# Performance work log

Hardware: AMD Instinct MI355X
Metric: run time of the kernel (lower is better)

The kernel has to match this reference:

```python
import jax, jax.numpy as jnp
import numpy as np

B, S, D, H = 2, 2048, 1024, 16
HD = D // H

def setup_inputs() -> dict:
    key = jax.random.key(0)
    ks = jax.random.split(key, 5)
    x = jax.random.normal(ks[0], (B, S, D), dtype=jnp.float32)
    scale = float(np.sqrt(6.0 / (D + D)))  # xavier_uniform bound
    def xavier(k):
        return jax.random.uniform(k, (D, D), dtype=jnp.float32, minval=-scale, maxval=scale)
    WQ, WK, WV, WO = xavier(ks[1]), xavier(ks[2]), xavier(ks[3]), xavier(ks[4])
    # causal mask, 1 = valid, 0 = masked, shape (B, 1, S_q, S_k)
    mask = jnp.broadcast_to(jnp.tril(jnp.ones((S, S), dtype=jnp.int32)), (B, 1, S, S))
    return {"x": x, "WQ": WQ, "WK": WK, "WV": WV, "WO": WO, "mask": mask}

def reference(x, WQ, WK, WV, WO, mask):
    b, s, d = x.shape
    # projections and head split: (B, H, S, HD)
    def split_heads(t):
        return t.reshape(b, s, H, HD).transpose(0, 2, 1, 3)
    q = split_heads(x @ WQ)
    k = split_heads(x @ WK)
    v = split_heads(x @ WV)
    scores = jnp.einsum('bhqd,bhkd->bhqk', q, k) / jnp.sqrt(jnp.float32(HD))
    neg = jnp.finfo(scores.dtype).min
    scores = jnp.where(mask == 0, neg, scores)
    attn = jax.nn.softmax(scores, axis=-1)
    out = jnp.einsum('bhqk,bhkd->bhqd', attn, v)  # (B, H, S, HD)
    out = out.transpose(0, 2, 1, 3).reshape(b, s, d)
    return out @ WO
```

## Files before the change

### kernel.cpp

```cpp
#include <hip/hip_runtime.h>
#include <hip/hip_bf16.h>


typedef __attribute__((ext_vector_type(8))) short short8;
typedef __attribute__((ext_vector_type(4))) float floatx4;
typedef __attribute__((ext_vector_type(4))) unsigned short ushort4v;
typedef __attribute__((ext_vector_type(2))) unsigned int uint2v;

#define GLDS16(gp, lp) __builtin_amdgcn_global_load_lds( \
    (const __attribute__((address_space(1))) void*)(gp), \
    (__attribute__((address_space(3))) void*)(lp), 16, 0, 0)

#define EXP2F(x) __builtin_amdgcn_exp2f(x)
#define NEG_INF (-__builtin_inff())

__device__ __forceinline__ unsigned short f2bf(float f) {
  unsigned int u = __builtin_bit_cast(unsigned int, f);
  return (unsigned short)((u + 0x7fffu + ((u >> 16) & 1u)) >> 16);
}
__device__ __forceinline__ float bf2f(unsigned short h) {
  unsigned int u = ((unsigned int)h) << 16;
  return __builtin_bit_cast(float, u);
}
__device__ __forceinline__ unsigned int pack2bf(float a, float b) {
#if __has_builtin(__builtin_amdgcn_cvt_pk_bf16_f32)
  auto r = __builtin_amdgcn_cvt_pk_bf16_f32(a, b);
  return __builtin_bit_cast(unsigned int, r);
#else
  unsigned int ua = (__builtin_bit_cast(unsigned int, a) + 0x8000u) >> 16;
  unsigned int ub = (__builtin_bit_cast(unsigned int, b) + 0x8000u) & 0xFFFF0000u;
  return ua | ub;
#endif
}
__device__ __forceinline__ floatx4 mfma16(short8 a, short8 b, floatx4 c) {
  return __builtin_amdgcn_mfma_f32_16x16x32_bf16(a, b, c, 0, 0, 0);
}

__global__ void k_convert_x(const float* __restrict__ x, unsigned short* __restrict__ xb) {
  int i = (blockIdx.x * 256 + threadIdx.x) * 4;
  ushort4v o;
  o.x = f2bf(x[i + 0]);
  o.y = f2bf(x[i + 1]);
  o.z = f2bf(x[i + 2]);
  o.w = f2bf(x[i + 3]);
  *(ushort4v*)(xb + i) = o;
}

__global__ void k_transpose_w(const float* __restrict__ WQ, const float* __restrict__ WK,
                              const float* __restrict__ WV, const float* __restrict__ WO,
                              unsigned short* __restrict__ wtq, unsigned short* __restrict__ wto,
                              int* __restrict__ counter) {
  if (threadIdx.x == 0 && blockIdx.x == 0 && blockIdx.y == 0 && blockIdx.z == 0) *counter = 0;
  __shared__ float tile[32][33];
  const float* W = (blockIdx.z == 0) ? WQ : (blockIdx.z == 1) ? WK : (blockIdx.z == 2) ? WV : WO;
  unsigned short* dst = (blockIdx.z < 3) ? (wtq + (size_t)blockIdx.z * 1024 * 1024) : wto;
  int tx = threadIdx.x & 31, ty = threadIdx.x >> 5;
  int bx = blockIdx.x, by = blockIdx.y;
#pragma unroll
  for (int j = 0; j < 4; ++j)
    tile[ty + j * 8][tx] = W[(size_t)(by * 32 + ty + j * 8) * 1024 + bx * 32 + tx];
  __syncthreads();
#pragma unroll
  for (int j = 0; j < 4; ++j)
    dst[(size_t)(bx * 32 + ty + j * 8) * 1024 + by * 32 + tx] = f2bf(tile[tx][ty + j * 8]);
}

template <int MODE>
__global__ __launch_bounds__(256, 2) void k_gemm(
    const unsigned short* __restrict__ A, const unsigned short* __restrict__ BT,
    float* __restrict__ Cf, unsigned short* __restrict__ Qp,
    unsigned short* __restrict__ Kp, unsigned short* __restrict__ Vt, int K) {
  __shared__ __align__(16) unsigned short smem[128 * 136];
  unsigned short* lA = smem;
  unsigned short* lB = smem + 128 * 64;
  const int tid = threadIdx.x;
  const int wave = tid >> 6, lane = tid & 63;
  const int wm = wave & 1, wn = wave >> 1;
  const int m0 = blockIdx.x * 128, n0 = blockIdx.y * 128;
  const int l15 = lane & 15, l16 = lane >> 4;
  const int r8 = lane >> 3, c8 = lane & 7;
  const int gchunk = (c8 ^ r8) << 3;

  floatx4 acc[4][4] = {};
  for (int k0 = 0; k0 < K; k0 += 64) {
    __syncthreads();
#pragma unroll
    for (int i = 0; i < 4; ++i) {
      int seg = wave * 4 + i;
      int row = seg * 8 + r8;
      GLDS16(A + (size_t)(m0 + row) * K + k0 + gchunk, lA + seg * 512);
      GLDS16(BT + (size_t)(n0 + row) * K + k0 + gchunk, lB + seg * 512);
    }
    __syncthreads();
#pragma unroll
    for (int ks = 0; ks < 2; ++ks) {
      short8 af[4], bfr[4];
#pragma unroll
      for (int t = 0; t < 4; ++t) {
        int m = wm * 64 + t * 16 + l15;
        int cl = ks * 4 + l16;
        af[t] = *(const short8*)(lA + m * 64 + ((cl ^ (m & 7)) << 3));
        int n = wn * 64 + t * 16 + l15;
        bfr[t] = *(const short8*)(lB + n * 64 + ((cl ^ (n & 7)) << 3));
      }
#pragma unroll
      for (int mt = 0; mt < 4; ++mt)
#pragma unroll
        for (int nt = 0; nt < 4; ++nt)
          acc[mt][nt] = mfma16(af[mt], bfr[nt], acc[mt][nt]);
    }
  }
  const int sel = n0 >> 10;
  if (MODE == 1) {
#pragma unroll
    for (int mt = 0; mt < 4; ++mt)
#pragma unroll
      for (int nt = 0; nt < 4; ++nt)
#pragma unroll
        for (int r = 0; r < 4; ++r) {
          int m = m0 + wm * 64 + mt * 16 + l16 * 4 + r;
          int n = n0 + wn * 64 + nt * 16 + l15;
          Cf[(size_t)m * 1024 + n] = acc[mt][nt][r];
        }
  } else if (sel < 2) {
    unsigned short* dst = (sel == 0) ? Qp : Kp;
    __syncthreads();
#pragma unroll
    for (int mt = 0; mt < 4; ++mt)
#pragma unroll
      for (int nt = 0; nt < 4; ++nt)
#pragma unroll
        for (int r = 0; r < 4; ++r) {
          int ml = wm * 64 + mt * 16 + l16 * 4 + r;
          int nl = wn * 64 + nt * 16 + l15;
          smem[ml * 136 + nl] = f2bf(acc[mt][nt][r]);
        }
    __syncthreads();
    const int b = m0 >> 11, s0 = m0 & 2047;
    const int h0 = (n0 & 1023) >> 6;
#pragma unroll
    for (int it = 0; it < 8; ++it) {
      int ml = it * 16 + (tid >> 4);
      int c = (tid & 15) * 8;
      short8 v = *(const short8*)(smem + ml * 136 + c);
      int h = h0 + (c >> 6), hd = c & 63;
      *(short8*)(dst + ((size_t)((b * 16 + h) * 2048 + s0 + ml) << 6) + hd) = v;
    }
  } else {
    __syncthreads();
#pragma unroll
    for (int mt = 0; mt < 4; ++mt)
#pragma unroll
      for (int nt = 0; nt < 4; ++nt)
#pragma unroll
        for (int r = 0; r < 4; ++r) {
          int nl = wn * 64 + nt * 16 + l15;
          int ml = wm * 64 + mt * 16 + l16 * 4 + r;
          smem[nl * 136 + ml] = f2bf(acc[mt][nt][r]);
        }
    __syncthreads();
    const int b = m0 >> 11, s0 = m0 & 2047;
    const int h0 = (n0 - 2048) >> 6;
#pragma unroll
    for (int it = 0; it < 8; ++it) {
      int nl = it * 16 + (tid >> 4);
      int sc = (tid & 15) * 8;
      short8 v = *(const short8*)(smem + nl * 136 + sc);
      int hh = h0 + (nl >> 6), hd = nl & 63;
      *(short8*)(Vt + ((size_t)(b * 16 + hh) * 64 + hd) * 2048 + s0 + sc) = v;
    }
  }
}

__global__ __launch_bounds__(256, 2) void k_attn(
    const unsigned short* __restrict__ Qp, const unsigned short* __restrict__ Kp,
    const unsigned short* __restrict__ Vt, float* __restrict__ Opart,
    float* __restrict__ lpart, int* __restrict__ counter) {
  __shared__ __align__(16) unsigned short kvbuf[2][2][64 * 64];
  __shared__ __align__(16) unsigned short pbuf[4][32 * 64];
  __shared__ int sjob;
  const int tid = threadIdx.x, wave = tid >> 6, lane = tid & 63;
  const int l15 = lane & 15, l16 = lane >> 4;
  const int r8 = lane >> 3, c8 = lane & 7;
  const int gchunk = (c8 ^ r8) << 3;
  unsigned short* pb = &pbuf[wave][0];
  const float qscale = 0.125f * 1.44269504088896f;
  short8 onesv;
#pragma unroll
  for (int j = 0; j < 8; ++j) onesv[j] = (short)0x3F80;

#define STAGE(KT, BUF) \
  { _Pragma("unroll") for (int i_ = 0; i_ < 2; ++i_) { \
      int seg_ = wave * 2 + i_; \
      GLDS16(Kp + base + (size_t)((KT) * 64 + seg_ * 8 + r8) * 64 + gchunk, \
             &kvbuf[BUF][0][0] + seg_ * 512); \
      GLDS16(Vt + base + (size_t)(seg_ * 8 + r8) * 2048 + (KT) * 64 + gchunk, \
             &kvbuf[BUF][1][0] + seg_ * 512); \
    } }

  for (;;) {
    __syncthreads();
    if (tid == 0) sjob = atomicAdd(counter, 1);
    __syncthreads();
    const int job = sjob;
    if (job >= 1024) break;
    const int qt = 15 - (job >> 6);
    const int half = (job >> 5) & 1;
    const int bh = job & 31;
    const int kt0 = half ? (qt + 1) : 0;
    const int kt1 = half ? (2 * qt + 2) : (qt + 1);
    const int R0 = qt * 128 + wave * 32;
    const size_t base = (size_t)bh << 17;

    short8 qf[2][2];
#pragma unroll
    for (int mt = 0; mt < 2; ++mt)
#pragma unroll
      for (int ks = 0; ks < 2; ++ks) {
        short8 v = *(const short8*)(Qp + base + (size_t)(R0 + mt * 16 + l15) * 64 +
                                    ks * 32 + l16 * 8);
#pragma unroll
        for (int j = 0; j < 8; ++j) {
          float f = bf2f((unsigned short)v[j]) * qscale;
          v[j] = (short)f2bf(f);
        }
        qf[mt][ks] = v;
      }

    floatx4 oacc[4][2] = {};
    floatx4 lacc[2] = {};

    STAGE(kt0, 0);
    for (int kt = kt0; kt < kt1; ++kt) {
      const int cb = (kt - kt0) & 1;
      __syncthreads();
      if (kt + 1 < kt1) STAGE(kt + 1, cb ^ 1);
      if (kt * 64 > R0 + 31) continue;
      const unsigned short* kb = &kvbuf[cb][0][0];
      const unsigned short* vb = &kvbuf[cb][1][0];

      floatx4 sacc[2][4] = {};
#pragma unroll
      for (int ks = 0; ks < 2; ++ks) {
        short8 kfr[4];
#pragma unroll
        for (int nt = 0; nt < 4; ++nt) {
          int row = nt * 16 + l15;
          int cl = ks * 4 + l16;
          kfr[nt] = *(const short8*)(kb + row * 64 + ((cl ^ (row & 7)) << 3));
        }
#pragma unroll
        for (int mt = 0; mt < 2; ++mt)
#pragma unroll
          for (int nt = 0; nt < 4; ++nt)
            sacc[mt][nt] = mfma16(kfr[nt], qf[mt][ks], sacc[mt][nt]);
      }
      if (kt * 64 + 63 > R0) {
#pragma unroll
        for (int mt = 0; mt < 2; ++mt)
#pragma unroll
          for (int nt = 0; nt < 4; ++nt)
#pragma unroll
            for (int rr = 0; rr < 4; ++rr) {
              int key = kt * 64 + nt * 16 + l16 * 4 + rr;
              int qrow = R0 + mt * 16 + l15;
              if (key > qrow) sacc[mt][nt][rr] = NEG_INF;
            }
      }
#pragma unroll
      for (int mt = 0; mt < 2; ++mt)
#pragma unroll
        for (int nt = 0; nt < 4; ++nt) {
          uint2v pk;
          pk.x = pack2bf(EXP2F(sacc[mt][nt][0]), EXP2F(sacc[mt][nt][1]));
          pk.y = pack2bf(EXP2F(sacc[mt][nt][2]), EXP2F(sacc[mt][nt][3]));
          int q = mt * 16 + l15;
          int ch = (nt * 4 + l16) ^ ((q & 7) << 1);
          *(uint2v*)(pb + q * 64 + ch * 4) = pk;
        }
      short8 pfr[2][2];
#pragma unroll
      for (int mt = 0; mt < 2; ++mt)
#pragma unroll
        for (int ks = 0; ks < 2; ++ks) {
          int q = mt * 16 + l15;
          int ch = (ks * 8 + l16 * 2) ^ ((q & 7) << 1);
          pfr[mt][ks] = *(const short8*)(pb + q * 64 + ch * 4);
        }
#pragma unroll
      for (int ks = 0; ks < 2; ++ks) {
        short8 vf[4];
#pragma unroll
        for (int ht = 0; ht < 4; ++ht) {
          int row = ht * 16 + l15;
          int cl = ks * 4 + l16;
          vf[ht] = *(const short8*)(vb + row * 64 + ((cl ^ (row & 7)) << 3));
        }
#pragma unroll
        for (int mt = 0; mt < 2; ++mt) {
          lacc[mt] = mfma16(onesv, pfr[mt][ks], lacc[mt]);
#pragma unroll
          for (int ht = 0; ht < 4; ++ht)
            oacc[ht][mt] = mfma16(vf[ht], pfr[mt][ks], oacc[ht][mt]);
        }
      }
    }

    float* Os = Opart + (size_t)job * 8192;
#pragma unroll
    for (int ht = 0; ht < 4; ++ht)
#pragma unroll
      for (int mt = 0; mt < 2; ++mt) {
        int ql = wave * 32 + mt * 16 + l15;
#pragma unroll
        for (int r = 0; r < 4; ++r) {
          int hd = ht * 16 + l16 * 4 + r;
          Os[(size_t)hd * 128 + ql] = oacc[ht][mt][r];
        }
      }
    if (l16 == 0) {
      lpart[job * 128 + wave * 32 + l15] = lacc[0][0];
      lpart[job * 128 + wave * 32 + 16 + l15] = lacc[1][0];
    }
  }
#undef STAGE
}

__global__ __launch_bounds__(256, 2) void k_comb(
    const float* __restrict__ Opart, const float* __restrict__ lpart,
    unsigned short* __restrict__ Ob) {
  __shared__ float lds[32][129];
  __shared__ float linv[128];
  const int tid = threadIdx.x;
  const int qt = 15 - (blockIdx.x >> 5);
  const int bh = blockIdx.x & 31;
  const int jA = ((blockIdx.x >> 5) << 6) | bh;
  const int jB = jA + 32;
  const float* Oa = Opart + (size_t)jA * 8192;
  const float* Op2 = Opart + (size_t)jB * 8192;
  if (tid < 128) linv[tid] = 1.0f / (lpart[jA * 128 + tid] + lpart[jB * 128 + tid]);
  const int b = bh >> 4, h = bh & 15;
  const size_t obase = ((size_t)(b * 2048 + qt * 128)) * 1024 + h * 64;
#pragma unroll
  for (int c = 0; c < 2; ++c) {
    __syncthreads();
#pragma unroll
    for (int i = 0; i < 16; ++i) {
      int hdl = i * 2 + (tid >> 7);
      int rl = tid & 127;
      size_t off = (size_t)(c * 32 + hdl) * 128 + rl;
      lds[hdl][rl] = Oa[off] + Op2[off];
    }
    __syncthreads();
#pragma unroll
    for (int i = 0; i < 16; ++i) {
      int rl = i * 8 + (tid >> 5);
      int hdl = tid & 31;
      float v = lds[hdl][rl] * linv[rl];
      Ob[obase + (size_t)rl * 1024 + c * 32 + hdl] = f2bf(v);
    }
  }
}

extern "C" void kernel_launch(void* const* d_in, const int* in_sizes, int n_in,
                              void* d_out, int out_size, void* d_ws, size_t ws_size,
                              hipStream_t stream) {
  const float* x = (const float*)d_in[0];
  const float* WQ = (const float*)d_in[1];
  const float* WK = (const float*)d_in[2];
  const float* WV = (const float*)d_in[3];
  const float* WO = (const float*)d_in[4];
  float* out = (float*)d_out;
  char* ws = (char*)d_ws;
  unsigned short* xb = (unsigned short*)(ws);
  unsigned short* wtq = (unsigned short*)(ws + 8388608);
  unsigned short* wto = (unsigned short*)(ws + 14680064);
  unsigned short* Qp = (unsigned short*)(ws + 16777216);
  unsigned short* Kp = (unsigned short*)(ws + 25165824);
  unsigned short* Vt = (unsigned short*)(ws + 33554432);
  unsigned short* Ob = (unsigned short*)(ws + 41943040);
  int* counter = (int*)(ws + 50331648);
  float* Opart = (float*)(ws + 50335744);
  float* lpart = (float*)(ws + 83890176);

  k_convert_x<<<dim3(4096), dim3(256), 0, stream>>>(x, xb);
  k_transpose_w<<<dim3(32, 32, 4), dim3(256), 0, stream>>>(WQ, WK, WV, WO, wtq, wto, counter);
  k_gemm<0><<<dim3(32, 24), dim3(256), 0, stream>>>(xb, wtq, (float*)nullptr, Qp, Kp, Vt, 1024);
  k_attn<<<dim3(512), dim3(256), 0, stream>>>(Qp, Kp, Vt, Opart, lpart, counter);
  k_comb<<<dim3(512), dim3(256), 0, stream>>>(Opart, lpart, Ob);
  k_gemm<1><<<dim3(32, 8), dim3(256), 0, stream>>>(Ob, wto, out, (unsigned short*)nullptr,
                                                   (unsigned short*)nullptr,
                                                   (unsigned short*)nullptr, 1024);
}
```

Baseline: 197.0 us.

## Fuse prep kernels, store attention partials as bf16, and shard job queue by XCD

Merges the x conversion and weight transpose into one launch. The attention job counter is split into 8 per-queue counters keyed on blockIdx.x & 7, which groups head work per XCD and cuts atomic contention. Partial outputs are written as bf16 in row-major layout, so the combine kernel does vectorized loads without an LDS transpose. This halves partial-buffer traffic at the cost of an extra bf16 rounding before the two halves are summed.

```diff
diff --git a/kernel.cpp b/kernel.cpp
--- a/kernel.cpp
+++ b/kernel.cpp
@@ -36,33 +36,37 @@
   return __builtin_amdgcn_mfma_f32_16x16x32_bf16(a, b, c, 0, 0, 0);
 }
 
-__global__ void k_convert_x(const float* __restrict__ x, unsigned short* __restrict__ xb) {
-  int i = (blockIdx.x * 256 + threadIdx.x) * 4;
-  ushort4v o;
-  o.x = f2bf(x[i + 0]);
-  o.y = f2bf(x[i + 1]);
-  o.z = f2bf(x[i + 2]);
-  o.w = f2bf(x[i + 3]);
-  *(ushort4v*)(xb + i) = o;
-}
-
-__global__ void k_transpose_w(const float* __restrict__ WQ, const float* __restrict__ WK,
-                              const float* __restrict__ WV, const float* __restrict__ WO,
-                              unsigned short* __restrict__ wtq, unsigned short* __restrict__ wto,
-                              int* __restrict__ counter) {
-  if (threadIdx.x == 0 && blockIdx.x == 0 && blockIdx.y == 0 && blockIdx.z == 0) *counter = 0;
-  __shared__ float tile[32][33];
-  const float* W = (blockIdx.z == 0) ? WQ : (blockIdx.z == 1) ? WK : (blockIdx.z == 2) ? WV : WO;
-  unsigned short* dst = (blockIdx.z < 3) ? (wtq + (size_t)blockIdx.z * 1024 * 1024) : wto;
-  int tx = threadIdx.x & 31, ty = threadIdx.x >> 5;
-  int bx = blockIdx.x, by = blockIdx.y;
-#pragma unroll
-  for (int j = 0; j < 4; ++j)
-    tile[ty + j * 8][tx] = W[(size_t)(by * 32 + ty + j * 8) * 1024 + bx * 32 + tx];
-  __syncthreads();
-#pragma unroll
-  for (int j = 0; j < 4; ++j)
-    dst[(size_t)(bx * 32 + ty + j * 8) * 1024 + by * 32 + tx] = f2bf(tile[tx][ty + j * 8]);
+__global__ void k_prep(const float* __restrict__ x, unsigned short* __restrict__ xb,
+                       const float* __restrict__ WQ, const float* __restrict__ WK,
+                       const float* __restrict__ WV, const float* __restrict__ WO,
+                       unsigned short* __restrict__ wtq, unsigned short* __restrict__ wto,
+                       int* __restrict__ counters) {
+  const int z = blockIdx.z;
+  if (z < 4) {
+    if (z == 0 && blockIdx.x == 0 && blockIdx.y == 0 && threadIdx.x < 8)
+      counters[threadIdx.x] = 0;
+    __shared__ float tile[32][33];
+    const float* W = (z == 0) ? WQ : (z == 1) ? WK : (z == 2) ? WV : WO;
+    unsigned short* dst = (z < 3) ? (wtq + (size_t)z * 1024 * 1024) : wto;
+    int tx = threadIdx.x & 31, ty = threadIdx.x >> 5;
+    int bx = blockIdx.x, by = blockIdx.y;
+#pragma unroll
+    for (int j = 0; j < 4; ++j)
+      tile[ty + j * 8][tx] = W[(size_t)(by * 32 + ty + j * 8) * 1024 + bx * 32 + tx];
+    __syncthreads();
+#pragma unroll
+    for (int j = 0; j < 4; ++j)
+      dst[(size_t)(bx * 32 + ty + j * 8) * 1024 + by * 32 + tx] = f2bf(tile[tx][ty + j * 8]);
+  } else {
+    int fi = (((z - 4) * 1024 + blockIdx.y * 32 + blockIdx.x) << 8) + threadIdx.x;
+    int i = fi * 4;
+    ushort4v o;
+    o.x = f2bf(x[i + 0]);
+    o.y = f2bf(x[i + 1]);
+    o.z = f2bf(x[i + 2]);
+    o.w = f2bf(x[i + 3]);
+    *(ushort4v*)(xb + i) = o;
+  }
 }
 
 template <int MODE>
@@ -174,12 +178,13 @@
 
 __global__ __launch_bounds__(256, 2) void k_attn(
     const unsigned short* __restrict__ Qp, const unsigned short* __restrict__ Kp,
-    const unsigned short* __restrict__ Vt, float* __restrict__ Opart,
-    float* __restrict__ lpart, int* __restrict__ counter) {
+    const unsigned short* __restrict__ Vt, unsigned short* __restrict__ Opart,
+    float* __restrict__ lpart, int* __restrict__ counters) {
   __shared__ __align__(16) unsigned short kvbuf[2][2][64 * 64];
   __shared__ __align__(16) unsigned short pbuf[4][32 * 64];
   __shared__ int sjob;
   const int tid = threadIdx.x, wave = tid >> 6, lane = tid & 63;
+  const int q = blockIdx.x & 7;
   const int l15 = lane & 15, l16 = lane >> 4;
   const int r8 = lane >> 3, c8 = lane & 7;
   const int gchunk = (c8 ^ r8) << 3;
@@ -200,13 +205,14 @@
 
   for (;;) {
     __syncthreads();
-    if (tid == 0) sjob = atomicAdd(counter, 1);
-    __syncthreads();
-    const int job = sjob;
-    if (job >= 1024) break;
-    const int qt = 15 - (job >> 6);
-    const int half = (job >> 5) & 1;
-    const int bh = job & 31;
+    if (tid == 0) sjob = atomicAdd(&counters[q], 1);
+    __syncthreads();
+    const int jq = sjob;
+    if (jq >= 128) break;
+    const int qt = 15 - (jq >> 3);
+    const int half = jq & 1;
+    const int bh = q | (((jq >> 1) & 3) << 3);
+    const int slot = jq * 8 + q;
     const int kt0 = half ? (qt + 1) : 0;
     const int kt1 = half ? (2 * qt + 2) : (qt + 1);
     const int R0 = qt * 128 + wave * 32;
@@ -274,18 +280,18 @@
           uint2v pk;
           pk.x = pack2bf(EXP2F(sacc[mt][nt][0]), EXP2F(sacc[mt][nt][1]));
           pk.y = pack2bf(EXP2F(sacc[mt][nt][2]), EXP2F(sacc[mt][nt][3]));
-          int q = mt * 16 + l15;
-          int ch = (nt * 4 + l16) ^ ((q & 7) << 1);
-          *(uint2v*)(pb + q * 64 + ch * 4) = pk;
+          int qq = mt * 16 + l15;
+          int ch = (nt * 4 + l16) ^ ((qq & 7) << 1);
+          *(uint2v*)(pb + qq * 64 + ch * 4) = pk;
         }
       short8 pfr[2][2];
 #pragma unroll
       for (int mt = 0; mt < 2; ++mt)
 #pragma unroll
         for (int ks = 0; ks < 2; ++ks) {
-          int q = mt * 16 + l15;
-          int ch = (ks * 8 + l16 * 2) ^ ((q & 7) << 1);
-          pfr[mt][ks] = *(const short8*)(pb + q * 64 + ch * 4);
+          int qq = mt * 16 + l15;
+          int ch = (ks * 8 + l16 * 2) ^ ((qq & 7) << 1);
+          pfr[mt][ks] = *(const short8*)(pb + qq * 64 + ch * 4);
         }
 #pragma unroll
       for (int ks = 0; ks < 2; ++ks) {
@@ -306,59 +312,59 @@
       }
     }
 
-    float* Os = Opart + (size_t)job * 8192;
+    unsigned short* Os = Opart + (size_t)slot * 8192;
 #pragma unroll
     for (int ht = 0; ht < 4; ++ht)
 #pragma unroll
       for (int mt = 0; mt < 2; ++mt) {
         int ql = wave * 32 + mt * 16 + l15;
-#pragma unroll
-        for (int r = 0; r < 4; ++r) {
-          int hd = ht * 16 + l16 * 4 + r;
-          Os[(size_t)hd * 128 + ql] = oacc[ht][mt][r];
-        }
+        uint2v pk;
+        pk.x = pack2bf(oacc[ht][mt][0], oacc[ht][mt][1]);
+        pk.y = pack2bf(oacc[ht][mt][2], oacc[ht][mt][3]);
+        *(uint2v*)(Os + ql * 64 + ht * 16 + l16 * 4) = pk;
       }
     if (l16 == 0) {
-      lpart[job * 128 + wave * 32 + l15] = lacc[0][0];
-      lpart[job * 128 + wave * 32 + 16 + l15] = lacc[1][0];
+      lpart[slot * 128 + wave * 32 + l15] = lacc[0][0];
+      lpart[slot * 128 + wave * 32 + 16 + l15] = lacc[1][0];
     }
   }
 #undef STAGE
 }
 
 __global__ __launch_bounds__(256, 2) void k_comb(
-    const float* __restrict__ Opart, const float* __restrict__ lpart,
+    const unsigned short* __restrict__ Opart, const float* __restrict__ lpart,
     unsigned short* __restrict__ Ob) {
-  __shared__ float lds[32][129];
   __shared__ float linv[128];
   const int tid = threadIdx.x;
-  const int qt = 15 - (blockIdx.x >> 5);
+  const int qtIdx = blockIdx.x >> 5;
+  const int qt = 15 - qtIdx;
   const int bh = blockIdx.x & 31;
-  const int jA = ((blockIdx.x >> 5) << 6) | bh;
-  const int jB = jA + 32;
-  const float* Oa = Opart + (size_t)jA * 8192;
-  const float* Op2 = Opart + (size_t)jB * 8192;
-  if (tid < 128) linv[tid] = 1.0f / (lpart[jA * 128 + tid] + lpart[jB * 128 + tid]);
+  const int q = bh & 7, bhl = bh >> 3;
+  const int jqA = qtIdx * 8 + bhl * 2;
+  const int sA = jqA * 8 + q, sB = (jqA + 1) * 8 + q;
+  const unsigned short* A = Opart + (size_t)sA * 8192;
+  const unsigned short* Bp = Opart + (size_t)sB * 8192;
+  if (tid < 128) linv[tid] = 1.0f / (lpart[sA * 128 + tid] + lpart[sB * 128 + tid]);
+  __syncthreads();
   const int b = bh >> 4, h = bh & 15;
   const size_t obase = ((size_t)(b * 2048 + qt * 128)) * 1024 + h * 64;
 #pragma unroll
-  for (int c = 0; c < 2; ++c) {
-    __syncthreads();
-#pragma unroll
-    for (int i = 0; i < 16; ++i) {
-      int hdl = i * 2 + (tid >> 7);
-      int rl = tid & 127;
-      size_t off = (size_t)(c * 32 + hdl) * 128 + rl;
-      lds[hdl][rl] = Oa[off] + Op2[off];
-    }
-    __syncthreads();
-#pragma unroll
-    for (int i = 0; i < 16; ++i) {
-      int rl = i * 8 + (tid >> 5);
-      int hdl = tid & 31;
-      float v = lds[hdl][rl] * linv[rl];
-      Ob[obase + (size_t)rl * 1024 + c * 32 + hdl] = f2bf(v);
-    }
+  for (int k = 0; k < 4; ++k) {
+    int o = k * 2048 + tid * 8;
+    int ql = o >> 6, hd = o & 63;
+    short8 a = *(const short8*)(A + o);
+    short8 c = *(const short8*)(Bp + o);
+    float iv = linv[ql];
+    short8 r;
+#pragma unroll
+    for (int j = 0; j < 8; j += 2) {
+      unsigned int pk = pack2bf(
+          (bf2f((unsigned short)a[j]) + bf2f((unsigned short)c[j])) * iv,
+          (bf2f((unsigned short)a[j + 1]) + bf2f((unsigned short)c[j + 1])) * iv);
+      r[j] = (short)(pk & 0xFFFF);
+      r[j + 1] = (short)(pk >> 16);
+    }
+    *(short8*)(Ob + obase + (size_t)ql * 1024 + hd) = r;
   }
 }
 
@@ -379,14 +385,13 @@
   unsigned short* Kp = (unsigned short*)(ws + 25165824);
   unsigned short* Vt = (unsigned short*)(ws + 33554432);
   unsigned short* Ob = (unsigned short*)(ws + 41943040);
-  int* counter = (int*)(ws + 50331648);
-  float* Opart = (float*)(ws + 50335744);
-  float* lpart = (float*)(ws + 83890176);
-
-  k_convert_x<<<dim3(4096), dim3(256), 0, stream>>>(x, xb);
-  k_transpose_w<<<dim3(32, 32, 4), dim3(256), 0, stream>>>(WQ, WK, WV, WO, wtq, wto, counter);
+  int* counters = (int*)(ws + 50331648);
+  unsigned short* Opart = (unsigned short*)(ws + 50335744);
+  float* lpart = (float*)(ws + 67112960);
+
+  k_prep<<<dim3(32, 32, 8), dim3(256), 0, stream>>>(x, xb, WQ, WK, WV, WO, wtq, wto, counters);
   k_gemm<0><<<dim3(32, 24), dim3(256), 0, stream>>>(xb, wtq, (float*)nullptr, Qp, Kp, Vt, 1024);
-  k_attn<<<dim3(512), dim3(256), 0, stream>>>(Qp, Kp, Vt, Opart, lpart, counter);
+  k_attn<<<dim3(512), dim3(256), 0, stream>>>(Qp, Kp, Vt, Opart, lpart, counters);
   k_comb<<<dim3(512), dim3(256), 0, stream>>>(Opart, lpart, Ob);
   k_gemm<1><<<dim3(32, 8), dim3(256), 0, stream>>>(Ob, wto, out, (unsigned short*)nullptr,
                                                    (unsigned short*)nullptr,
```

Result: no change. 193.2 us (-1.9%).
